# Performance work log

Hardware: AMD Instinct MI355X
Metric: run time of the kernel (lower is better)

## Reference

```python
import jax, jax.numpy as jnp
import numpy as np

B, W, KD, NC, D, NN, NH, AD, HOPS = 512, 4, 64, 32, 256, 16, 8, 32, 4
DH = D // NH
DFF = 4 * D
P = B * W + B
ROLE_WRITER, ROLE_QUERY = 0, 1


def setup_inputs() -> dict:
    key = jax.random.key(0)
    ks = iter(jax.random.split(key, 40))
    f = lambda shape, s=0.02: jax.random.normal(next(ks), shape, dtype=jnp.float32) * s
    inp = {
        'query_keys': jax.random.normal(next(ks), (B, KD), dtype=jnp.float32),
        'writer_keys': jax.random.normal(next(ks), (B, W, KD), dtype=jnp.float32),
        'key_proj_w': f((KD, D)), 'key_proj_b': jnp.zeros((D,), jnp.float32),
        'class_embed': f((NC, D)), 'role_embed': f((3, D)), 'start_node_embed': f((NN, D)),
        'input_ln_g': jnp.ones((D,), jnp.float32), 'input_ln_b': jnp.zeros((D,), jnp.float32),
        'ln1_g': jnp.ones((NN, D), jnp.float32), 'ln1_b': jnp.zeros((NN, D), jnp.float32),
        'wqkv': f((NN, D, 3 * D)), 'bqkv': jnp.zeros((NN, 3 * D), jnp.float32),
        'wo': f((NN, D, D)), 'bo': jnp.zeros((NN, D), jnp.float32),
        'ln2_g': jnp.ones((NN, D), jnp.float32), 'ln2_b': jnp.zeros((NN, D), jnp.float32),
        'w_fc1': f((NN, D, DFF)), 'b_fc1': jnp.zeros((NN, DFF), jnp.float32),
        'w_fc2': f((NN, DFF, D)), 'b_fc2': jnp.zeros((NN, D), jnp.float32),
        'delta_w': jnp.zeros((D, D), jnp.float32), 'delta_b': jnp.zeros((D,), jnp.float32),
        'dir_w': f((D, D)), 'dir_b': jnp.zeros((D,), jnp.float32),
        'mag_w': f((D, 1)), 'mag_b': jnp.full((1,), 2.5, jnp.float32),
        'out_w': f((D, NC)), 'out_b': jnp.zeros((NC,), jnp.float32),
        'address_table': jax.random.normal(next(ks), (NN, AD), dtype=jnp.float32),
        'query_start_nodes': jax.random.randint(next(ks), (B,), 0, NN),
        'writer_labels': jax.random.randint(next(ks), (B, W), 0, NC),
        'writer_start_nodes': jax.random.randint(next(ks), (B, W), 0, NN),
    }
    return inp


def _ln(x):
    m = jnp.mean(x, -1, keepdims=True)
    v = jnp.var(x, -1, keepdims=True)
    return (x - m) * jax.lax.rsqrt(v + 1e-5)


def _forward(query_keys, writer_keys, key_proj_w, key_proj_b, class_embed, role_embed,
             start_node_embed, input_ln_g, input_ln_b, ln1_g, ln1_b, wqkv, bqkv, wo, bo,
             ln2_g, ln2_b, w_fc1, b_fc1, w_fc2, b_fc2, delta_w, delta_b, dir_w, dir_b,
             mag_w, mag_b, out_w, out_b, address_table,
             query_start_nodes, writer_labels, writer_start_nodes):
    # ---- encode writers (encode_writers) ----
    fk = writer_keys.reshape(-1, KD)          # [B*W, KD]
    fl = writer_labels.reshape(-1)            # [B*W]
    fs = writer_start_nodes.reshape(-1)       # [B*W]
    learned_w = fk @ key_proj_w + key_proj_b + class_embed[fl] + start_node_embed[fs] + role_embed[ROLE_WRITER]
    sw = jnp.zeros_like(learned_w).at[:, :KD].set(fk)
    sw = sw.at[:, KD:KD + NC].set(jax.nn.one_hot(fl, NC, dtype=learned_w.dtype))
    enc_w = _ln(learned_w) * input_ln_g + input_ln_b + sw
    # ---- encode queries (encode_queries) ----
    learned_q = query_keys @ key_proj_w + key_proj_b + start_node_embed[query_start_nodes] + role_embed[ROLE_QUERY]
    sq = jnp.zeros_like(learned_q).at[:, :KD].set(query_keys)
    enc_q = _ln(learned_q) * input_ln_g + input_ln_b + sq

    h = jnp.concatenate([enc_w, enc_q], axis=0)          # [P, D]
    node = jnp.concatenate([fs, query_start_nodes], 0)   # [P] current compute node per packet

    inv_sqrt_dh = 1.0 / np.sqrt(DH).astype(np.float32)
    for _ in range(HOPS):
        oh = jax.nn.one_hot(node, NN, dtype=h.dtype)      # [P, NN] dispatch weights

        def pnl(x, Wn, bn):
            # per-node linear: gather-compute-scatter via MoE-style dense dispatch
            xe = jnp.einsum('pn,pd->npd', oh, x)          # [NN, P, din]
            ye = jnp.einsum('npd,ndf->npf', xe, Wn)       # [NN, P, dout]
            return jnp.einsum('npf,pn->pf', ye, oh) + oh @ bn

        # ComputeNodeCell: pre-LN attention among packets at the same node
        x = _ln(h) * (oh @ ln1_g) + oh @ ln1_b
        qkv = pnl(x, wqkv, bqkv)                          # [P, 3D]
        q, k, v = jnp.split(qkv, 3, axis=-1)
        q = q.reshape(P, NH, DH); k = k.reshape(P, NH, DH); v = v.reshape(P, NH, DH)
        scores = jnp.einsum('phd,qhd->hpq', q, k) * inv_sqrt_dh   # [NH, P, P]
        same = node[:, None] == node[None, :]
        scores = jnp.where(same[None], scores, -1e9)
        attn = jax.nn.softmax(scores, axis=-1)
        ao = jnp.einsum('hpq,qhd->phd', attn, v).reshape(P, D)
        h = h + pnl(ao, wo, bo)
        # MLP block
        x2 = _ln(h) * (oh @ ln2_g) + oh @ ln2_b
        h = h + pnl(jax.nn.gelu(pnl(x2, w_fc1, b_fc1)), w_fc2, b_fc2)
        # routing heads: pick next node from address table, apply gated delta
        direction = h @ dir_w + dir_b
        node = jnp.argmax(direction[:, :AD] @ address_table.T, axis=-1)
        h = h + (h @ delta_w + delta_b) * jax.nn.sigmoid(h @ mag_w + mag_b)

    return h @ out_w + out_b                              # [P, NC] per-packet logits


def reference(query_keys, writer_keys, key_proj_w, key_proj_b, class_embed, role_embed,
              start_node_embed, input_ln_g, input_ln_b, ln1_g, ln1_b, wqkv, bqkv, wo, bo,
              ln2_g, ln2_b, w_fc1, b_fc1, w_fc2, b_fc2, delta_w, delta_b, dir_w, dir_b,
              mag_w, mag_b, out_w, out_b, address_table,
              query_start_nodes, writer_labels, writer_start_nodes):
    return _forward(query_keys, writer_keys, key_proj_w, key_proj_b, class_embed, role_embed,
                    start_node_embed, input_ln_g, input_ln_b, ln1_g, ln1_b, wqkv, bqkv, wo, bo,
                    ln2_g, ln2_b, w_fc1, b_fc1, w_fc2, b_fc2, delta_w, delta_b, dir_w, dir_b,
                    mag_w, mag_b, out_w, out_b, address_table,
                    query_start_nodes, writer_labels, writer_start_nodes)
```

## Files before the change

### kernel.cpp

```cpp
#include <hip/hip_runtime.h>
#include <math.h>

#define B_    512
#define W_    4
#define KD_   64
#define NC_   32
#define D_    256
#define NN_   16
#define NH_   8
#define AD_   32
#define HOPS_ 4
#define DH_   32
#define DFF_  1024
#define P_    2560
#define BW_   2048
#define MAXT_ 56

#define INV_SQRT_DH 0.17677669529663687f

__device__ __forceinline__ float block_sum256(float v, float* red) {
#pragma unroll
  for (int off = 32; off > 0; off >>= 1) v += __shfl_xor(v, off, 64);
  int wid = threadIdx.x >> 6;
  if ((threadIdx.x & 63) == 0) red[wid] = v;
  __syncthreads();
  float s = red[0] + red[1] + red[2] + red[3];
  __syncthreads();
  return s;
}

__device__ __forceinline__ float gelu_tanh(float v) {
  float u = 0.7978845608028654f * (v + 0.044715f * v * v * v);
  return 0.5f * v * (1.0f + tanhf(u));
}

__global__ __launch_bounds__(256) void encode_kernel(
    const float* __restrict__ query_keys, const float* __restrict__ writer_keys,
    const float* __restrict__ kpw, const float* __restrict__ kpb,
    const float* __restrict__ ce, const float* __restrict__ re,
    const float* __restrict__ sne, const float* __restrict__ ilg,
    const float* __restrict__ ilb, const int* __restrict__ qsn,
    const int* __restrict__ wl, const int* __restrict__ wsn,
    float* __restrict__ h, int* __restrict__ node) {
  int p = blockIdx.x, t = threadIdx.x;
  __shared__ float fk[KD_];
  __shared__ float red[4];
  const float* key;
  int lab = -1, sn, role;
  if (p < BW_) { key = writer_keys + (size_t)p * KD_; lab = wl[p]; sn = wsn[p]; role = 0; }
  else { int b = p - BW_; key = query_keys + (size_t)b * KD_; sn = qsn[b]; role = 1; }
  if (t < KD_) fk[t] = key[t];
  __syncthreads();

  float acc = kpb[t] + sne[sn * D_ + t] + re[role * D_ + t];
  if (lab >= 0) acc += ce[lab * D_ + t];
#pragma unroll 8
  for (int i = 0; i < KD_; i++) acc += fk[i] * kpw[i * D_ + t];

  float mean = block_sum256(acc, red) * (1.0f / D_);
  float d = acc - mean;
  float var = block_sum256(d * d, red) * (1.0f / D_);
  float xn = d * (1.0f / sqrtf(var + 1e-5f));

  float sw = 0.0f;
  if (t < KD_) sw = fk[t];
  else if (lab >= 0 && t < KD_ + NC_) sw = (t - KD_ == lab) ? 1.0f : 0.0f;

  h[(size_t)p * D_ + t] = xn * ilg[t] + ilb[t] + sw;
  if (t == 0) node[p] = sn;
}

__global__ __launch_bounds__(256) void sort_kernel(const int* __restrict__ node,
                                                   int* __restrict__ order,
                                                   int* __restrict__ offs,
                                                   int* __restrict__ cnts,
                                                   int* __restrict__ tnode,
                                                   int* __restrict__ tstart,
                                                   int* __restrict__ tend,
                                                   int* __restrict__ ntiles) {
  __shared__ int c[NN_], o[NN_], cur[NN_];
  int t = threadIdx.x;
  if (t < NN_) c[t] = 0;
  __syncthreads();
  for (int p = t; p < P_; p += 256) atomicAdd(&c[node[p]], 1);
  __syncthreads();
  if (t == 0) {
    int s = 0;
    for (int n = 0; n < NN_; n++) { o[n] = s; cur[n] = s; s += c[n]; }
    int idx = 0;
    for (int n = 0; n < NN_; n++) {
      int e = o[n] + c[n];
      for (int m0 = o[n]; m0 < e; m0 += 64) {
        tnode[idx] = n; tstart[idx] = m0; tend[idx] = e; idx++;
      }
    }
    ntiles[0] = idx;
  }
  __syncthreads();
  if (t < NN_) { cnts[t] = c[t]; offs[t] = o[t]; }
  for (int p = t; p < P_; p += 256) {
    int r = atomicAdd(&cur[node[p]], 1);
    order[r] = p;
  }
}

__global__ __launch_bounds__(256) void ln_affine(const float* __restrict__ h,
                                                 const float* __restrict__ g,
                                                 const float* __restrict__ b,
                                                 const int* __restrict__ node,
                                                 const int* __restrict__ order,
                                                 float* __restrict__ x) {
  int sp = blockIdx.x, t = threadIdx.x;
  __shared__ float red[4];
  int p = order[sp];
  int n = node[p];
  float v = h[(size_t)p * D_ + t];
  float mean = block_sum256(v, red) * (1.0f / D_);
  float d = v - mean;
  float var = block_sum256(d * d, red) * (1.0f / D_);
  float xn = d * (1.0f / sqrtf(var + 1e-5f));
  x[(size_t)sp * D_ + t] = xn * g[n * D_ + t] + b[n * D_ + t];
}

template <int DIN, int DOUT, int ACT, int RESID, int PER_NODE>
__global__ __launch_bounds__(256) void glin(const float* __restrict__ x,
                                            const float* __restrict__ W,
                                            const float* __restrict__ bias,
                                            float* __restrict__ out,
                                            const int* __restrict__ order,
                                            const int* __restrict__ tnode,
                                            const int* __restrict__ tstart,
                                            const int* __restrict__ tend,
                                            const int* __restrict__ ntiles) {
  constexpr int KC = 32, STX = 68;
  constexpr int NCH = DIN / KC;
  int ti = blockIdx.x;
  int n, s0, s1;
  if (PER_NODE) {
    if (ti >= ntiles[0]) return;
    n = tnode[ti]; s0 = tstart[ti]; s1 = tend[ti];
  } else {
    n = 0; s0 = ti * 64; s1 = P_;
  }
  int jbase = blockIdx.y * 64;
  int rows = s1 - s0; if (rows > 64) rows = 64;

  __shared__ float xs[2][KC][STX];
  __shared__ float ws[2][KC][64];

  int tid = threadIdx.x;
  const float* Wn = W + (size_t)n * DIN * DOUT + jbase;

  int xrow = tid >> 2, xq = tid & 3;
  bool xvalid = xrow < rows;
  const float* xptr = x + (size_t)(s0 + (xvalid ? xrow : 0)) * DIN + xq * 4;

  float4 xr0, xr1;
  auto xfetch = [&](int kc) {
    if (xvalid) {
      xr0 = *(const float4*)(xptr + kc);
      xr1 = *(const float4*)(xptr + kc + 16);
    } else {
      xr0 = make_float4(0.f, 0.f, 0.f, 0.f);
      xr1 = make_float4(0.f, 0.f, 0.f, 0.f);
    }
  };
  auto xstage = [&](int buf) {
    xs[buf][xq * 4 + 0][xrow] = xr0.x;
    xs[buf][xq * 4 + 1][xrow] = xr0.y;
    xs[buf][xq * 4 + 2][xrow] = xr0.z;
    xs[buf][xq * 4 + 3][xrow] = xr0.w;
    xs[buf][xq * 4 + 16][xrow] = xr1.x;
    xs[buf][xq * 4 + 17][xrow] = xr1.y;
    xs[buf][xq * 4 + 18][xrow] = xr1.z;
    xs[buf][xq * 4 + 19][xrow] = xr1.w;
  };
  int wvw = tid >> 6, lane = tid & 63;
  auto wfetch = [&](int buf, int kc) {
#pragma unroll
    for (int i = 0; i < 2; i++) {
      int kr = wvw * 8 + i * 4;
      const float* g = &Wn[(size_t)(kc + kr + (lane >> 4)) * DOUT + (lane & 15) * 4];
      __builtin_amdgcn_global_load_lds(
          (const __attribute__((address_space(1))) unsigned int*)g,
          (__attribute__((address_space(3))) unsigned int*)&ws[buf][kr][0],
          16, 0, 0);
    }
  };

  wfetch(0, 0);
  xfetch(0);
  xstage(0);
  __syncthreads();

  int rc4 = (tid >> 4) * 4;
  int jc4 = (tid & 15) * 4;
  float acc[4][4] = {{0.f}};

  for (int c = 0; c < NCH; c++) {
    int cur = c & 1;
    if (c + 1 < NCH) {
      wfetch(cur ^ 1, (c + 1) * KC);
      xfetch((c + 1) * KC);
    }
#pragma unroll 8
    for (int k = 0; k < KC; k++) {
      float4 a = *(const float4*)&xs[cur][k][rc4];
      float4 b = *(const float4*)&ws[cur][k][jc4];
      acc[0][0] += a.x * b.x; acc[0][1] += a.x * b.y; acc[0][2] += a.x * b.z; acc[0][3] += a.x * b.w;
      acc[1][0] += a.y * b.x; acc[1][1] += a.y * b.y; acc[1][2] += a.y * b.z; acc[1][3] += a.y * b.w;
      acc[2][0] += a.z * b.x; acc[2][1] += a.z * b.y; acc[2][2] += a.z * b.z; acc[2][3] += a.z * b.w;
      acc[3][0] += a.w * b.x; acc[3][1] += a.w * b.y; acc[3][2] += a.w * b.z; acc[3][3] += a.w * b.w;
    }
    if (c + 1 < NCH) xstage(cur ^ 1);
    __syncthreads();
  }

  float4 bb = *(const float4*)&bias[n * DOUT + jbase + jc4];
#pragma unroll
  for (int r = 0; r < 4; r++) {
    int lr = rc4 + r;
    if (lr >= rows) continue;
    float v[4];
    v[0] = acc[r][0] + bb.x; v[1] = acc[r][1] + bb.y;
    v[2] = acc[r][2] + bb.z; v[3] = acc[r][3] + bb.w;
    if (ACT == 1) {
      v[0] = gelu_tanh(v[0]); v[1] = gelu_tanh(v[1]);
      v[2] = gelu_tanh(v[2]); v[3] = gelu_tanh(v[3]);
    }
    if (RESID) {
      int pp = PER_NODE ? order[s0 + lr] : (s0 + lr);
      float* op = &out[(size_t)pp * DOUT + jbase + jc4];
      float4 old = *(const float4*)op;
      *(float4*)op = make_float4(v[0] + old.x, v[1] + old.y, v[2] + old.z, v[3] + old.w);
    } else {
      float* op = &out[(size_t)(s0 + lr) * DOUT + jbase + jc4];
      *(float4*)op = make_float4(v[0], v[1], v[2], v[3]);
    }
  }
}

#define ATS 36
__global__ __launch_bounds__(256) void attn_kernel(const float* __restrict__ qkv,
                                                   const int* __restrict__ node,
                                                   const int* __restrict__ order,
                                                   const int* __restrict__ offs,
                                                   const int* __restrict__ cnts,
                                                   float* __restrict__ ao) {
  __shared__ float qs[32 * ATS];
  __shared__ float kts[32 * ATS];
  __shared__ float vs[32 * ATS];
  __shared__ float ps[32 * ATS];
  __shared__ int glo[32], ghi[32];

  int t = threadIdx.x;
  int r = t >> 3;
  int j4 = (t & 7) * 4;
  int r0 = blockIdx.x * 32;
  int hd = blockIdx.y;

  if (t < 32) {
    int n = node[order[r0 + t]];
    glo[t] = offs[n];
    ghi[t] = offs[n] + cnts[n];
  }
  __syncthreads();

  {
    const float* qp = &qkv[(size_t)(r0 + r) * 768 + hd * 32 + j4];
    float4 q4 = *(const float4*)qp;
    q4.x *= INV_SQRT_DH; q4.y *= INV_SQRT_DH; q4.z *= INV_SQRT_DH; q4.w *= INV_SQRT_DH;
    *(float4*)&qs[r * ATS + j4] = q4;
  }

  int lo = glo[0];
  int hi = ghi[31];
  int myglo = glo[r], myghi = ghi[r];

  float4 o4 = {0.f, 0.f, 0.f, 0.f};
  float mrow = -1e30f, lrow = 0.f;

  for (int kt = lo; kt < hi; kt += 32) {
    int sj = kt + r;
    float4 k4 = {0.f, 0.f, 0.f, 0.f}, v4 = {0.f, 0.f, 0.f, 0.f};
    if (sj < hi) {
      const float* kp = &qkv[(size_t)sj * 768 + 256 + hd * 32 + j4];
      k4 = *(const float4*)kp;
      v4 = *(const float4*)(kp + 256);
    }
    __syncthreads();
    kts[(j4 + 0) * ATS + r] = k4.x;
    kts[(j4 + 1) * ATS + r] = k4.y;
    kts[(j4 + 2) * ATS + r] = k4.z;
    kts[(j4 + 3) * ATS + r] = k4.w;
    *(float4*)&vs[r * ATS + j4] = v4;
    __syncthreads();

    float s0 = 0.f, s1 = 0.f, s2 = 0.f, s3 = 0.f;
#pragma unroll 8
    for (int d = 0; d < 32; d++) {
      float qv = qs[r * ATS + d];
      float4 kv = *(const float4*)&kts[d * ATS + j4];
      s0 += qv * kv.x; s1 += qv * kv.y; s2 += qv * kv.z; s3 += qv * kv.w;
    }
    int c0 = kt + j4;
    if (c0 + 0 < myglo || c0 + 0 >= myghi) s0 = -1e30f;
    if (c0 + 1 < myglo || c0 + 1 >= myghi) s1 = -1e30f;
    if (c0 + 2 < myglo || c0 + 2 >= myghi) s2 = -1e30f;
    if (c0 + 3 < myglo || c0 + 3 >= myghi) s3 = -1e30f;

    float mx = fmaxf(fmaxf(s0, s1), fmaxf(s2, s3));
#pragma unroll
    for (int off = 4; off > 0; off >>= 1) mx = fmaxf(mx, __shfl_xor(mx, off, 8));
    float mnew = fmaxf(mrow, mx);
    float alpha = __expf(mrow - mnew);
    float p0 = __expf(s0 - mnew), p1 = __expf(s1 - mnew);
    float p2 = __expf(s2 - mnew), p3 = __expf(s3 - mnew);
    float ls = p0 + p1 + p2 + p3;
#pragma unroll
    for (int off = 4; off > 0; off >>= 1) ls += __shfl_xor(ls, off, 8);
    lrow = lrow * alpha + ls;
    mrow = mnew;
    o4.x *= alpha; o4.y *= alpha; o4.z *= alpha; o4.w *= alpha;

    *(float4*)&ps[r * ATS + j4] = make_float4(p0, p1, p2, p3);
#pragma unroll 8
    for (int j = 0; j < 32; j++) {
      float pj = ps[r * ATS + j];
      float4 vv = *(const float4*)&vs[j * ATS + j4];
      o4.x += pj * vv.x; o4.y += pj * vv.y; o4.z += pj * vv.z; o4.w += pj * vv.w;
    }
  }

  float inv = 1.f / lrow;
  o4.x *= inv; o4.y *= inv; o4.z *= inv; o4.w *= inv;
  *(float4*)&ao[(size_t)(r0 + r) * D_ + hd * 32 + j4] = o4;
}

__global__ __launch_bounds__(256) void route_kernel(float* __restrict__ h,
                                                    const float* __restrict__ dir_w,
                                                    const float* __restrict__ dir_b,
                                                    const float* __restrict__ at,
                                                    const float* __restrict__ mag_w,
                                                    const float* __restrict__ mag_b,
                                                    const float* __restrict__ delta,
                                                    int* __restrict__ node) {
  int p = blockIdx.x, t = threadIdx.x;
  __shared__ float hs[D_];
  __shared__ float dpart[8][AD_];
  __shared__ float dirs[AD_];
  __shared__ float scs[NN_];
  __shared__ float red[4];
  float hv = h[(size_t)p * D_ + t];
  hs[t] = hv;
  __syncthreads();

  int j = t & 31, seg = t >> 5;
  float part = 0.0f;
#pragma unroll 8
  for (int i = 0; i < 32; i++) {
    int ii = seg * 32 + i;
    part += hs[ii] * dir_w[ii * D_ + j];
  }
  dpart[seg][j] = part;
  __syncthreads();
  if (t < AD_) {
    float s = dir_b[t];
#pragma unroll
    for (int g = 0; g < 8; g++) s += dpart[g][t];
    dirs[t] = s;
  }
  __syncthreads();
  if (t < NN_) {
    float s = 0.0f;
#pragma unroll
    for (int a = 0; a < AD_; a++) s += dirs[a] * at[t * AD_ + a];
    scs[t] = s;
  }
  __syncthreads();
  if (t == 0) {
    float best = scs[0];
    int arg = 0;
    for (int nn = 1; nn < NN_; nn++)
      if (scs[nn] > best) { best = scs[nn]; arg = nn; }
    node[p] = arg;
  }
  float mag = block_sum256(hv * mag_w[t], red) + mag_b[0];
  float sig = 1.0f / (1.0f + __expf(-mag));
  h[(size_t)p * D_ + t] = hv + delta[(size_t)p * D_ + t] * sig;
}

__global__ __launch_bounds__(256) void out_kernel(const float* __restrict__ h,
                                                  const float* __restrict__ ow,
                                                  const float* __restrict__ ob,
                                                  float* __restrict__ out) {
  int p = blockIdx.x, t = threadIdx.x;
  __shared__ float hs[D_];
  __shared__ float part[8][NC_];
  hs[t] = h[(size_t)p * D_ + t];
  __syncthreads();
  int j = t & 31, seg = t >> 5;
  float s = 0.0f;
#pragma unroll 8
  for (int i = 0; i < 32; i++) {
    int ii = seg * 32 + i;
    s += hs[ii] * ow[ii * NC_ + j];
  }
  part[seg][j] = s;
  __syncthreads();
  if (t < NC_) {
    float r = ob[t];
#pragma unroll
    for (int g = 0; g < 8; g++) r += part[g][t];
    out[(size_t)p * NC_ + t] = r;
  }
}

extern "C" void kernel_launch(void* const* d_in, const int* in_sizes, int n_in,
                              void* d_out, int out_size, void* d_ws, size_t ws_size,
                              hipStream_t stream) {
  (void)in_sizes; (void)n_in; (void)out_size; (void)ws_size;
  const float* query_keys       = (const float*)d_in[0];
  const float* writer_keys      = (const float*)d_in[1];
  const float* key_proj_w       = (const float*)d_in[2];
  const float* key_proj_b       = (const float*)d_in[3];
  const float* class_embed      = (const float*)d_in[4];
  const float* role_embed       = (const float*)d_in[5];
  const float* start_node_embed = (const float*)d_in[6];
  const float* input_ln_g       = (const float*)d_in[7];
  const float* input_ln_b       = (const float*)d_in[8];
  const float* ln1_g            = (const float*)d_in[9];
  const float* ln1_b            = (const float*)d_in[10];
  const float* wqkv             = (const float*)d_in[11];
  const float* bqkv             = (const float*)d_in[12];
  const float* wo               = (const float*)d_in[13];
  const float* bo               = (const float*)d_in[14];
  const float* ln2_g            = (const float*)d_in[15];
  const float* ln2_b            = (const float*)d_in[16];
  const float* w_fc1            = (const float*)d_in[17];
  const float* b_fc1            = (const float*)d_in[18];
  const float* w_fc2            = (const float*)d_in[19];
  const float* b_fc2            = (const float*)d_in[20];
  const float* delta_w          = (const float*)d_in[21];
  const float* delta_b          = (const float*)d_in[22];
  const float* dir_w            = (const float*)d_in[23];
  const float* dir_b            = (const float*)d_in[24];
  const float* mag_w            = (const float*)d_in[25];
  const float* mag_b            = (const float*)d_in[26];
  const float* out_w            = (const float*)d_in[27];
  const float* out_b            = (const float*)d_in[28];
  const float* address_table    = (const float*)d_in[29];
  const int* query_start_nodes  = (const int*)d_in[30];
  const int* writer_labels      = (const int*)d_in[31];
  const int* writer_start_nodes = (const int*)d_in[32];

  uintptr_t basep = (uintptr_t)d_ws;
  auto carve = [&](size_t bytes) {
    basep = (basep + 255) & ~(uintptr_t)255;
    void* r = (void*)basep;
    basep += bytes;
    return r;
  };
  float* h    = (float*)carve((size_t)P_ * D_ * 4);
  float* x    = (float*)carve((size_t)P_ * D_ * 4);
  float* qkvb = (float*)carve((size_t)P_ * 3 * D_ * 4);
  float* ff   = (float*)carve((size_t)P_ * DFF_ * 4);
  int* node   = (int*)carve(P_ * 4);
  int* order  = (int*)carve(P_ * 4);
  int* offs   = (int*)carve(NN_ * 4);
  int* cnts   = (int*)carve(NN_ * 4);
  int* tnode  = (int*)carve(MAXT_ * 4);
  int* tstart = (int*)carve(MAXT_ * 4);
  int* tend   = (int*)carve(MAXT_ * 4);
  int* ntiles = (int*)carve(4);

  encode_kernel<<<P_, 256, 0, stream>>>(query_keys, writer_keys, key_proj_w, key_proj_b,
                                        class_embed, role_embed, start_node_embed,
                                        input_ln_g, input_ln_b, query_start_nodes,
                                        writer_labels, writer_start_nodes, h, node);

  for (int hop = 0; hop < HOPS_; ++hop) {
    sort_kernel<<<1, 256, 0, stream>>>(node, order, offs, cnts,
                                       tnode, tstart, tend, ntiles);
    ln_affine<<<P_, 256, 0, stream>>>(h, ln1_g, ln1_b, node, order, x);
    glin<256, 768, 0, 0, 1><<<dim3(MAXT_, 12), 256, 0, stream>>>(
        x, wqkv, bqkv, qkvb, order, tnode, tstart, tend, ntiles);
    attn_kernel<<<dim3(P_ / 32, NH_), 256, 0, stream>>>(qkvb, node, order, offs, cnts,
                                                        x );
    glin<256, 256, 0, 1, 1><<<dim3(MAXT_, 4), 256, 0, stream>>>(
        x, wo, bo, h, order, tnode, tstart, tend, ntiles);
    ln_affine<<<P_, 256, 0, stream>>>(h, ln2_g, ln2_b, node, order, x);
    glin<256, 1024, 1, 0, 1><<<dim3(MAXT_, 16), 256, 0, stream>>>(
        x, w_fc1, b_fc1, ff, order, tnode, tstart, tend, ntiles);
    glin<1024, 256, 0, 1, 1><<<dim3(MAXT_, 4), 256, 0, stream>>>(
        ff, w_fc2, b_fc2, h, order, tnode, tstart, tend, ntiles);
    glin<256, 256, 0, 0, 0><<<dim3(P_ / 64, 4), 256, 0, stream>>>(
        h, delta_w, delta_b, qkvb , order,
        tnode, tstart, tend, ntiles);
    route_kernel<<<P_, 256, 0, stream>>>(h, dir_w, dir_b, address_table, mag_w, mag_b,
                                         qkvb, node);
  }

  out_kernel<<<P_, 256, 0, stream>>>(h, out_w, out_b, (float*)d_out);
}
```

Measured before the change: 993.0 us.

## Widen GEMM output tiles to 128 columns and split-K the FC2 projection

Adds a column-tile template parameter so the QKV, FC1 and FC2 grouped GEMMs use 64x128 tiles, with each thread computing 4x8 outputs. This gives more reuse of each loaded x value and halves the number of blocks along the output dimension. FC2 also gains a two-way K split: the second half writes partial sums to a new buffer, and a separate reduce kernel adds them into h. The cost is higher register pressure, an extra kernel launch, and extra global traffic for the partial buffer.

```diff
diff --git a/kernel.cpp b/kernel.cpp
--- a/kernel.cpp
+++ b/kernel.cpp
@@ -122,18 +122,24 @@
   x[(size_t)sp * D_ + t] = xn * g[n * D_ + t] + b[n * D_ + t];
 }
 
-template <int DIN, int DOUT, int ACT, int RESID, int PER_NODE>
+template <int DIN, int DOUT, int JT, int ACT, int RESID, int PER_NODE, int KSPLIT>
 __global__ __launch_bounds__(256) void glin(const float* __restrict__ x,
                                             const float* __restrict__ W,
                                             const float* __restrict__ bias,
                                             float* __restrict__ out,
+                                            float* __restrict__ pbuf,
                                             const int* __restrict__ order,
                                             const int* __restrict__ tnode,
                                             const int* __restrict__ tstart,
                                             const int* __restrict__ tend,
                                             const int* __restrict__ ntiles) {
   constexpr int KC = 32, STX = 68;
-  constexpr int NCH = DIN / KC;
+  constexpr int CPT = JT / 16;
+  constexpr int KLEN = DIN / KSPLIT;
+  constexpr int NCH = KLEN / KC;
+  constexpr int LPR = JT / 4;
+  constexpr int RPI = 64 / LPR;
+
   int ti = blockIdx.x;
   int n, s0, s1;
   if (PER_NODE) {
@@ -142,18 +148,20 @@
   } else {
     n = 0; s0 = ti * 64; s1 = P_;
   }
-  int jbase = blockIdx.y * 64;
+  int jbase = blockIdx.y * JT;
+  int kz = (KSPLIT > 1) ? blockIdx.z : 0;
+  int k0 = kz * KLEN;
   int rows = s1 - s0; if (rows > 64) rows = 64;
 
   __shared__ float xs[2][KC][STX];
-  __shared__ float ws[2][KC][64];
+  __shared__ float ws[2][KC][JT];
 
   int tid = threadIdx.x;
   const float* Wn = W + (size_t)n * DIN * DOUT + jbase;
 
   int xrow = tid >> 2, xq = tid & 3;
   bool xvalid = xrow < rows;
-  const float* xptr = x + (size_t)(s0 + (xvalid ? xrow : 0)) * DIN + xq * 4;
+  const float* xptr = x + (size_t)(s0 + (xvalid ? xrow : 0)) * DIN + k0 + xq * 4;
 
   float4 xr0, xr1;
   auto xfetch = [&](int kc) {
@@ -176,11 +184,13 @@
     xs[buf][xq * 4 + 19][xrow] = xr1.w;
   };
   int wvw = tid >> 6, lane = tid & 63;
+  int wlr = lane / LPR;
+  int wlc = (lane % LPR) * 4;
   auto wfetch = [&](int buf, int kc) {
 #pragma unroll
-    for (int i = 0; i < 2; i++) {
-      int kr = wvw * 8 + i * 4;
-      const float* g = &Wn[(size_t)(kc + kr + (lane >> 4)) * DOUT + (lane & 15) * 4];
+    for (int i = 0; i < 8 / RPI; i++) {
+      int kr = wvw * 8 + i * RPI;
+      const float* g = &Wn[(size_t)(k0 + kc + kr + wlr) * DOUT + wlc];
       __builtin_amdgcn_global_load_lds(
           (const __attribute__((address_space(1))) unsigned int*)g,
           (__attribute__((address_space(3))) unsigned int*)&ws[buf][kr][0],
@@ -193,9 +203,13 @@
   xstage(0);
   __syncthreads();
 
-  int rc4 = (tid >> 4) * 4;
-  int jc4 = (tid & 15) * 4;
-  float acc[4][4] = {{0.f}};
+  int r4 = (tid >> 4) * 4;
+  int jc = (tid & 15) * CPT;
+  float acc[4][CPT];
+#pragma unroll
+  for (int r = 0; r < 4; r++)
+#pragma unroll
+    for (int cc = 0; cc < CPT; cc++) acc[r][cc] = 0.f;
 
   for (int c = 0; c < NCH; c++) {
     int cur = c & 1;
@@ -205,39 +219,70 @@
     }
 #pragma unroll 8
     for (int k = 0; k < KC; k++) {
-      float4 a = *(const float4*)&xs[cur][k][rc4];
-      float4 b = *(const float4*)&ws[cur][k][jc4];
-      acc[0][0] += a.x * b.x; acc[0][1] += a.x * b.y; acc[0][2] += a.x * b.z; acc[0][3] += a.x * b.w;
-      acc[1][0] += a.y * b.x; acc[1][1] += a.y * b.y; acc[1][2] += a.y * b.z; acc[1][3] += a.y * b.w;
-      acc[2][0] += a.z * b.x; acc[2][1] += a.z * b.y; acc[2][2] += a.z * b.z; acc[2][3] += a.z * b.w;
-      acc[3][0] += a.w * b.x; acc[3][1] += a.w * b.y; acc[3][2] += a.w * b.z; acc[3][3] += a.w * b.w;
+      float4 a = *(const float4*)&xs[cur][k][r4];
+      float av[4] = {a.x, a.y, a.z, a.w};
+      float bv[CPT];
+      float4 b0 = *(const float4*)&ws[cur][k][jc];
+      bv[0] = b0.x; bv[1] = b0.y; bv[2] = b0.z; bv[3] = b0.w;
+      if (CPT == 8) {
+        float4 b1 = *(const float4*)&ws[cur][k][jc + 4];
+        bv[4] = b1.x; bv[5] = b1.y; bv[6] = b1.z; bv[7] = b1.w;
+      }
+#pragma unroll
+      for (int r = 0; r < 4; r++)
+#pragma unroll
+        for (int cc = 0; cc < CPT; cc++) acc[r][cc] += av[r] * bv[cc];
     }
     if (c + 1 < NCH) xstage(cur ^ 1);
     __syncthreads();
   }
 
-  float4 bb = *(const float4*)&bias[n * DOUT + jbase + jc4];
+  bool main_part = (KSPLIT == 1) || (kz == 0);
+  float bbv[CPT];
+#pragma unroll
+  for (int cc = 0; cc < CPT; cc++) bbv[cc] = bias[n * DOUT + jbase + jc + cc];
+
 #pragma unroll
   for (int r = 0; r < 4; r++) {
-    int lr = rc4 + r;
+    int lr = r4 + r;
     if (lr >= rows) continue;
-    float v[4];
-    v[0] = acc[r][0] + bb.x; v[1] = acc[r][1] + bb.y;
-    v[2] = acc[r][2] + bb.z; v[3] = acc[r][3] + bb.w;
-    if (ACT == 1) {
-      v[0] = gelu_tanh(v[0]); v[1] = gelu_tanh(v[1]);
-      v[2] = gelu_tanh(v[2]); v[3] = gelu_tanh(v[3]);
-    }
-    if (RESID) {
-      int pp = PER_NODE ? order[s0 + lr] : (s0 + lr);
-      float* op = &out[(size_t)pp * DOUT + jbase + jc4];
-      float4 old = *(const float4*)op;
-      *(float4*)op = make_float4(v[0] + old.x, v[1] + old.y, v[2] + old.z, v[3] + old.w);
+    float v[CPT];
+    if (main_part) {
+#pragma unroll
+      for (int cc = 0; cc < CPT; cc++) {
+        v[cc] = acc[r][cc] + bbv[cc];
+        if (ACT == 1) v[cc] = gelu_tanh(v[cc]);
+      }
+      if (RESID) {
+        int pp = PER_NODE ? order[s0 + lr] : (s0 + lr);
+        float* op = &out[(size_t)pp * DOUT + jbase + jc];
+#pragma unroll
+        for (int cc = 0; cc < CPT; cc += 4) {
+          float4 old = *(const float4*)(op + cc);
+          *(float4*)(op + cc) =
+              make_float4(v[cc] + old.x, v[cc + 1] + old.y, v[cc + 2] + old.z, v[cc + 3] + old.w);
+        }
+      } else {
+        float* op = &out[(size_t)(s0 + lr) * DOUT + jbase + jc];
+#pragma unroll
+        for (int cc = 0; cc < CPT; cc += 4)
+          *(float4*)(op + cc) = make_float4(v[cc], v[cc + 1], v[cc + 2], v[cc + 3]);
+      }
     } else {
-      float* op = &out[(size_t)(s0 + lr) * DOUT + jbase + jc4];
-      *(float4*)op = make_float4(v[0], v[1], v[2], v[3]);
-    }
-  }
+      float* op = &pbuf[(size_t)(s0 + lr) * DOUT + jbase + jc];
+#pragma unroll
+      for (int cc = 0; cc < CPT; cc += 4)
+        *(float4*)(op + cc) = make_float4(acc[r][cc], acc[r][cc + 1], acc[r][cc + 2], acc[r][cc + 3]);
+    }
+  }
+}
+
+__global__ __launch_bounds__(256) void reduce_kernel(float* __restrict__ h,
+                                                     const float* __restrict__ pbuf,
+                                                     const int* __restrict__ order) {
+  int sp = blockIdx.x, t = threadIdx.x;
+  int p = order[sp];
+  h[(size_t)p * D_ + t] += pbuf[(size_t)sp * D_ + t];
 }
 
 #define ATS 36
@@ -465,6 +510,7 @@
   float* x    = (float*)carve((size_t)P_ * D_ * 4);
   float* qkvb = (float*)carve((size_t)P_ * 3 * D_ * 4);
   float* ff   = (float*)carve((size_t)P_ * DFF_ * 4);
+  float* pbuf = (float*)carve((size_t)P_ * D_ * 4);
   int* node   = (int*)carve(P_ * 4);
   int* order  = (int*)carve(P_ * 4);
   int* offs   = (int*)carve(NN_ * 4);
@@ -483,19 +529,20 @@
     sort_kernel<<<1, 256, 0, stream>>>(node, order, offs, cnts,
                                        tnode, tstart, tend, ntiles);
     ln_affine<<<P_, 256, 0, stream>>>(h, ln1_g, ln1_b, node, order, x);
-    glin<256, 768, 0, 0, 1><<<dim3(MAXT_, 12), 256, 0, stream>>>(
-        x, wqkv, bqkv, qkvb, order, tnode, tstart, tend, ntiles);
+    glin<256, 768, 128, 0, 0, 1, 1><<<dim3(MAXT_, 6), 256, 0, stream>>>(
+        x, wqkv, bqkv, qkvb, nullptr, order, tnode, tstart, tend, ntiles);
     attn_kernel<<<dim3(P_ / 32, NH_), 256, 0, stream>>>(qkvb, node, order, offs, cnts,
                                                         x );
-    glin<256, 256, 0, 1, 1><<<dim3(MAXT_, 4), 256, 0, stream>>>(
-        x, wo, bo, h, order, tnode, tstart, tend, ntiles);
+    glin<256, 256, 64, 0, 1, 1, 1><<<dim3(MAXT_, 4), 256, 0, stream>>>(
+        x, wo, bo, h, nullptr, order, tnode, tstart, tend, ntiles);
     ln_affine<<<P_, 256, 0, stream>>>(h, ln2_g, ln2_b, node, order, x);
-    glin<256, 1024, 1, 0, 1><<<dim3(MAXT_, 16), 256, 0, stream>>>(
-        x, w_fc1, b_fc1, ff, order, tnode, tstart, tend, ntiles);
-    glin<1024, 256, 0, 1, 1><<<dim3(MAXT_, 4), 256, 0, stream>>>(
-        ff, w_fc2, b_fc2, h, order, tnode, tstart, tend, ntiles);
-    glin<256, 256, 0, 0, 0><<<dim3(P_ / 64, 4), 256, 0, stream>>>(
-        h, delta_w, delta_b, qkvb , order,
+    glin<256, 1024, 128, 1, 0, 1, 1><<<dim3(MAXT_, 8), 256, 0, stream>>>(
+        x, w_fc1, b_fc1, ff, nullptr, order, tnode, tstart, tend, ntiles);
+    glin<1024, 256, 128, 0, 1, 1, 2><<<dim3(MAXT_, 2, 2), 256, 0, stream>>>(
+        ff, w_fc2, b_fc2, h, pbuf, order, tnode, tstart, tend, ntiles);
+    reduce_kernel<<<P_, 256, 0, stream>>>(h, pbuf, order);
+    glin<256, 256, 64, 0, 0, 0, 1><<<dim3(P_ / 64, 4), 256, 0, stream>>>(
+        h, delta_w, delta_b, qkvb , nullptr, order,
         tnode, tstart, tend, ntiles);
     route_kernel<<<P_, 256, 0, stream>>>(h, dir_w, dir_b, address_table, mag_w, mag_b,
                                          qkvb, node);
```

New measurement: 1.001 ms. No clear change (+0.8%).
